# Optimization experiments

Hardware: AMD Instinct MI355X
Metric: run time of the kernel (lower is better)

The kernel has to match this reference:

```python
import jax, jax.numpy as jnp
import numpy as np

LEARNING_RATE = 0.1  # obj.learning_rate


def setup_inputs() -> dict:
    key = jax.random.key(0)
    k1, k2, k3, k4 = jax.random.split(key, 4)
    B, F = 50000, 100
    n_stages, n_classes, depth = 200, 10, 6
    T = n_stages * n_classes          # 2000 trees total
    n_internal = 2**depth - 1         # 63
    n_leaves = 2**depth               # 64
    x = jax.random.normal(k1, (B, F), dtype=jnp.float32)
    thresholds = jax.random.normal(k2, (T, n_internal), dtype=jnp.float32)
    leaf_values = jax.random.normal(k3, (T, n_leaves), dtype=jnp.float32)
    features = jax.random.randint(k4, (T, n_internal), 0, F, dtype=jnp.int32)
    classes = jnp.arange(n_classes, dtype=jnp.int64)
    return {"x": x, "thresholds": thresholds, "leaf_values": leaf_values,
            "features": features, "classes": classes}


def reference(x, thresholds, leaf_values, features, classes):
    # FIL-style batched traversal of complete depth-d trees.
    # Node i's children are 2i+1 (x[f] <= thr) and 2i+2 (x[f] > thr),
    # matching sklearn decision-tree split semantics.
    B = x.shape[0]
    T, n_internal = thresholds.shape
    n_leaves = leaf_values.shape[1]
    depth = int(np.log2(n_leaves))
    n_classes = classes.shape[0]

    tr = jnp.arange(T)[None, :]                      # [1, T] tree ids
    idx = jnp.zeros((B, T), dtype=jnp.int32)         # current node per (sample, tree)
    for _ in range(depth):                           # fixed small unroll (tree depth)
        f = features[tr, idx]                        # [B, T] split feature ids
        t = thresholds[tr, idx]                      # [B, T] split thresholds
        xv = jnp.take_along_axis(x, f, axis=1)       # [B, T] gathered feature values
        idx = 2 * idx + 1 + (xv > t).astype(jnp.int32)
    leaf = idx - (n_leaves - 1)                      # [B, T] leaf index in [0, n_leaves)
    vals = leaf_values[tr, leaf]                     # [B, T] per-tree outputs

    # stages-major layout: tree t = stage*n_classes + class; sum stages * lr
    # (init_ == 'zero' -> init output is zeros)
    decisions = LEARNING_RATE * vals.reshape(B, -1, n_classes).sum(axis=1)  # [B, C]
    # deviance, multiclass: predict_log_proba = log_softmax(decision_function)
    log_proba = jax.nn.log_softmax(decisions, axis=-1)
    # forward() = predict() = classes[argmax proba]; we return the float
    # log-probabilities (the differentiable hot path); argmax/class lookup is
    # a trivial epilogue: classes[jnp.argmax(log_proba, -1)]
    return log_proba
```

## Files before the change

kernel.cpp:

```cpp
#include <hip/hip_runtime.h>

#define B_SAMPLES 50000
#define F_FEATS   100
#define T_TREES   2000
#define N_INTERNAL 63
#define N_LEAVES  64
#define DEPTH     6
#define N_CLASSES 10
#define LR        0.1f

#define BLK 128
#define TPG 40
#define NCHUNK 10
#define TREES_PER_CHUNK (T_TREES / NCHUNK)
#define GROUPS_PER_CHUNK (TREES_PER_CHUNK / TPG)
#define NODE_STRIDE 64
#define NSB ((B_SAMPLES + BLK - 1) / BLK)

__global__ __launch_bounds__(256) void pack_nodes_kernel(
    const float* __restrict__ thresholds,
    const int*   __restrict__ features,
    int2*        __restrict__ nodes)
{
    int e = blockIdx.x * 256 + threadIdx.x;
    if (e < T_TREES * N_INTERNAL) {
        int t = e / N_INTERNAL;
        int i = e - t * N_INTERNAL;
        nodes[t * NODE_STRIDE + i] = make_int2(features[e], __float_as_int(thresholds[e]));
    }
}

#define I2F __int_as_float
#define XS(f) xs[((f) << 7) + tid]

template<bool PARTIALS>
__global__ __launch_bounds__(BLK, 1) void forest_kernel(
    const float* __restrict__ x,
    const int2*  __restrict__ nodes,
    const float* __restrict__ leaves,
    float*       __restrict__ accum)
{
    __shared__ float xs[F_FEATS * BLK];
    const int tid   = threadIdx.x;
    const int chunk = blockIdx.x % NCHUNK;
    const int sb    = blockIdx.x / NCHUNK;
    const int b     = sb * BLK + tid;
    const bool valid = (b < B_SAMPLES);

    {
        const float4* xrow = reinterpret_cast<const float4*>(x + (size_t)b * F_FEATS);
        #pragma unroll
        for (int k = 0; k < F_FEATS / 4; ++k) {
            float4 v = valid ? xrow[k] : make_float4(0.f, 0.f, 0.f, 0.f);
            xs[(4 * k + 0) * BLK + tid] = v.x;
            xs[(4 * k + 1) * BLK + tid] = v.y;
            xs[(4 * k + 2) * BLK + tid] = v.z;
            xs[(4 * k + 3) * BLK + tid] = v.w;
        }
    }
    __syncthreads();

    float acc[N_CLASSES];
    #pragma unroll
    for (int c = 0; c < N_CLASSES; ++c) acc[c] = 0.f;

    const int2*  cnodes  = nodes  + (size_t)chunk * TREES_PER_CHUNK * NODE_STRIDE;
    const float* cleaves = leaves + (size_t)chunk * TREES_PER_CHUNK * N_LEAVES;

    #pragma unroll 1
    for (int g = 0; g < GROUPS_PER_CHUNK; ++g) {
        const int2*  nbase = cnodes  + (size_t)g * TPG * NODE_STRIDE;
        const float* lbase = cleaves + (size_t)g * TPG * N_LEAVES;

        int idx[TPG];
        #pragma unroll
        for (int j = 0; j < TPG; ++j) idx[j] = 0;

        #pragma unroll
        for (int lvl = 0; lvl < DEPTH; ++lvl) {
            int2 nd[TPG];
            #pragma unroll
            for (int j = 0; j < TPG; ++j)
                nd[j] = nbase[j * NODE_STRIDE + idx[j]];
            #pragma unroll
            for (int j = 0; j < TPG; ++j) {
                float xv  = XS(nd[j].x);
                float thr = I2F(nd[j].y);
                idx[j] += idx[j] + 1 + (xv > thr ? 1 : 0);
            }
        }
        #pragma unroll
        for (int j = 0; j < TPG; ++j) {
            float lv = lbase[j * N_LEAVES + (idx[j] - (N_LEAVES - 1))];
            acc[j % N_CLASSES] += lv;
        }
    }

    if (valid) {
        if (PARTIALS) {
            float2* p = reinterpret_cast<float2*>(
                accum + ((size_t)chunk * B_SAMPLES + b) * N_CLASSES);
            #pragma unroll
            for (int c = 0; c < N_CLASSES / 2; ++c)
                p[c] = make_float2(acc[2 * c], acc[2 * c + 1]);
        } else {
            #pragma unroll
            for (int c = 0; c < N_CLASSES; ++c)
                atomicAdd(&accum[(size_t)b * N_CLASSES + c], acc[c]);
        }
    }
}

template<bool PARTIALS>
__global__ __launch_bounds__(256) void softmax_kernel(
    const float* __restrict__ accum,
    float*       __restrict__ out)
{
    int b = blockIdx.x * 256 + threadIdx.x;
    if (b >= B_SAMPLES) return;

    float d[N_CLASSES];
    #pragma unroll
    for (int c = 0; c < N_CLASSES; ++c) d[c] = 0.f;

    if (PARTIALS) {
        for (int ch = 0; ch < NCHUNK; ++ch) {
            const float2* p = reinterpret_cast<const float2*>(
                accum + ((size_t)ch * B_SAMPLES + b) * N_CLASSES);
            #pragma unroll
            for (int c = 0; c < N_CLASSES / 2; ++c) {
                float2 v = p[c];
                d[2 * c]     += v.x;
                d[2 * c + 1] += v.y;
            }
        }
    } else {
        #pragma unroll
        for (int c = 0; c < N_CLASSES; ++c)
            d[c] = accum[(size_t)b * N_CLASSES + c];
    }

    #pragma unroll
    for (int c = 0; c < N_CLASSES; ++c) d[c] *= LR;
    float m = d[0];
    #pragma unroll
    for (int c = 1; c < N_CLASSES; ++c) m = fmaxf(m, d[c]);
    float ssum = 0.f;
    #pragma unroll
    for (int c = 0; c < N_CLASSES; ++c) ssum += expf(d[c] - m);
    float lse = logf(ssum);

    float2* o = reinterpret_cast<float2*>(out + (size_t)b * N_CLASSES);
    #pragma unroll
    for (int c = 0; c < N_CLASSES / 2; ++c)
        o[c] = make_float2(d[2 * c] - m - lse, d[2 * c + 1] - m - lse);
}

extern "C" void kernel_launch(void* const* d_in, const int* in_sizes, int n_in,
                              void* d_out, int out_size, void* d_ws, size_t ws_size,
                              hipStream_t stream) {
    const float* x          = (const float*)d_in[0];
    const float* thresholds = (const float*)d_in[1];
    const float* leaves     = (const float*)d_in[2];
    const int*   features   = (const int*)d_in[3];

    const size_t nodes_bytes    = (size_t)T_TREES * NODE_STRIDE * sizeof(int2);
    const size_t partials_bytes = (size_t)NCHUNK * B_SAMPLES * N_CLASSES * sizeof(float);
    const size_t accum_bytes    = (size_t)B_SAMPLES * N_CLASSES * sizeof(float);

    int2*  nodes  = (int2*)d_ws;
    float* accbuf = (float*)((char*)d_ws + nodes_bytes);
    const bool use_partials = (ws_size >= nodes_bytes + partials_bytes);

    {
        int total = T_TREES * N_INTERNAL;
        pack_nodes_kernel<<<(total + 255) / 256, 256, 0, stream>>>(thresholds, features, nodes);
    }

    if (use_partials) {
        forest_kernel<true><<<NSB * NCHUNK, BLK, 0, stream>>>(x, nodes, leaves, accbuf);
        softmax_kernel<true><<<(B_SAMPLES + 255) / 256, 256, 0, stream>>>(accbuf, (float*)d_out);
    } else {
        hipMemsetAsync(accbuf, 0, accum_bytes, stream);
        forest_kernel<false><<<NSB * NCHUNK, BLK, 0, stream>>>(x, nodes, leaves, accbuf);
        softmax_kernel<false><<<(B_SAMPLES + 255) / 256, 256, 0, stream>>>(accbuf, (float*)d_out);
    }
}
```

Before: 402.2 us.

## Software-pipeline tree traversal across tree quarters and reorder block-to-chunk mapping

Halves the trees per group from 40 to 20 and splits them into four quarters of five. The traversal becomes a 24-step software pipeline: LDS reads of feature values for the next quarter are issued while the current quarter compares and issues its next global node or leaf load. Block indexing now puts the sample block in the fast dimension and the chunk in the slow one, so concurrently running blocks share the same tree chunk in cache. The aim is to hide global node-load and LDS latency, at the cost of more pipeline bookkeeping and less parallelism per group.

```diff
diff --git a/kernel.cpp b/kernel.cpp
--- a/kernel.cpp
+++ b/kernel.cpp
@@ -10,7 +10,8 @@
 #define LR        0.1f
 
 #define BLK 128
-#define TPG 40
+#define TPG 20
+#define QS  5
 #define NCHUNK 10
 #define TREES_PER_CHUNK (T_TREES / NCHUNK)
 #define GROUPS_PER_CHUNK (TREES_PER_CHUNK / TPG)
@@ -42,8 +43,8 @@
 {
     __shared__ float xs[F_FEATS * BLK];
     const int tid   = threadIdx.x;
-    const int chunk = blockIdx.x % NCHUNK;
-    const int sb    = blockIdx.x / NCHUNK;
+    const int chunk = blockIdx.x / NSB;
+    const int sb    = blockIdx.x % NSB;
     const int b     = sb * BLK + tid;
     const bool valid = (b < B_SAMPLES);
 
@@ -69,31 +70,47 @@
 
     #pragma unroll 1
     for (int g = 0; g < GROUPS_PER_CHUNK; ++g) {
-        const int2*  nbase = cnodes  + (size_t)g * TPG * NODE_STRIDE;
-        const float* lbase = cleaves + (size_t)g * TPG * N_LEAVES;
-
-        int idx[TPG];
+        const int2*  nb = cnodes  + (size_t)g * TPG * NODE_STRIDE;
+        const float* lb = cleaves + (size_t)g * TPG * N_LEAVES;
+
+        int   idx[TPG];
+        int2  nd [TPG];
+        float xv [TPG];
+        float lf [TPG];
+
         #pragma unroll
         for (int j = 0; j < TPG; ++j) idx[j] = 0;
-
-        #pragma unroll
-        for (int lvl = 0; lvl < DEPTH; ++lvl) {
-            int2 nd[TPG];
-            #pragma unroll
-            for (int j = 0; j < TPG; ++j)
-                nd[j] = nbase[j * NODE_STRIDE + idx[j]];
-            #pragma unroll
-            for (int j = 0; j < TPG; ++j) {
-                float xv  = XS(nd[j].x);
-                float thr = I2F(nd[j].y);
-                idx[j] += idx[j] + 1 + (xv > thr ? 1 : 0);
+        #pragma unroll
+        for (int j = 0; j < TPG; ++j) nd[j] = nb[j * NODE_STRIDE];
+        #pragma unroll
+        for (int jj = 0; jj < QS; ++jj) xv[jj] = XS(nd[jj].x);
+
+        #pragma unroll
+        for (int s = 0; s < 24; ++s) {
+            {
+                const int s1 = s + 1, q2 = s1 & 3, l2 = s1 >> 2, o2 = q2 * QS;
+                if (l2 <= 5) {
+                    #pragma unroll
+                    for (int jj = 0; jj < QS; ++jj) {
+                        const int j = o2 + jj;
+                        xv[j] = XS(nd[j].x);
+                    }
+                }
             }
-        }
-        #pragma unroll
-        for (int j = 0; j < TPG; ++j) {
-            float lv = lbase[j * N_LEAVES + (idx[j] - (N_LEAVES - 1))];
-            acc[j % N_CLASSES] += lv;
-        }
+            {
+                const int q = s & 3, l = s >> 2, o = q * QS;
+                #pragma unroll
+                for (int jj = 0; jj < QS; ++jj) {
+                    const int j = o + jj;
+                    idx[j] += idx[j] + 1 + (xv[j] > I2F(nd[j].y) ? 1 : 0);
+                    if (l < 5) nd[j] = nb[j * NODE_STRIDE + idx[j]];
+                    else       lf[j] = lb[j * N_LEAVES + idx[j] - (N_LEAVES - 1)];
+                }
+            }
+        }
+
+        #pragma unroll
+        for (int j = 0; j < TPG; ++j) acc[j % N_CLASSES] += lf[j];
     }
 
     if (valid) {
```

Measured after the change: 390.1 us. 3.0% less time.

## Split each block's tree chunk across four waves sharing the staged samples

Applied to the files above, without the earlier changes.

Each block now has 512 threads: four groups of 128 threads share the same 128 staged samples in LDS, and each group walks a quarter of the chunk's trees. The per-thread tree group shrinks from 40 to 10, which lowers register pressure and raises the number of resident waves for latency hiding. Per-class partial sums from the four groups are reduced through LDS before the write. This adds two barriers and an LDS reduction, and the x staging is divided among the groups. Occupancy may still be capped by the 51 KB LDS tile per block.

```diff
diff --git a/kernel.cpp b/kernel.cpp
--- a/kernel.cpp
+++ b/kernel.cpp
@@ -9,13 +9,17 @@
 #define N_CLASSES 10
 #define LR        0.1f
 
-#define BLK 128
-#define TPG 40
+#define SAMP 128
+#define NW   4
+#define THREADS (SAMP * NW)
+#define TPG 10
 #define NCHUNK 10
 #define TREES_PER_CHUNK (T_TREES / NCHUNK)
-#define GROUPS_PER_CHUNK (TREES_PER_CHUNK / TPG)
+#define TREES_PER_QUARTER (TREES_PER_CHUNK / NW)
+#define NGROUPS (TREES_PER_QUARTER / TPG)
 #define NODE_STRIDE 64
-#define NSB ((B_SAMPLES + BLK - 1) / BLK)
+#define NSB ((B_SAMPLES + SAMP - 1) / SAMP)
+#define RED_PAD 11
 
 __global__ __launch_bounds__(256) void pack_nodes_kernel(
     const float* __restrict__ thresholds,
@@ -31,31 +35,33 @@
 }
 
 #define I2F __int_as_float
-#define XS(f) xs[((f) << 7) + tid]
+#define XS(f) xs[((f) << 7) + s]
 
 template<bool PARTIALS>
-__global__ __launch_bounds__(BLK, 1) void forest_kernel(
+__global__ __launch_bounds__(THREADS, 1) void forest_kernel(
     const float* __restrict__ x,
     const int2*  __restrict__ nodes,
     const float* __restrict__ leaves,
     float*       __restrict__ accum)
 {
-    __shared__ float xs[F_FEATS * BLK];
+    __shared__ float xs[F_FEATS * SAMP];
     const int tid   = threadIdx.x;
+    const int s     = tid & (SAMP - 1);
+    const int w     = tid >> 7;
     const int chunk = blockIdx.x % NCHUNK;
     const int sb    = blockIdx.x / NCHUNK;
-    const int b     = sb * BLK + tid;
+    const int b     = sb * SAMP + s;
     const bool valid = (b < B_SAMPLES);
 
     {
         const float4* xrow = reinterpret_cast<const float4*>(x + (size_t)b * F_FEATS);
         #pragma unroll
-        for (int k = 0; k < F_FEATS / 4; ++k) {
+        for (int k = w; k < F_FEATS / 4; k += NW) {
             float4 v = valid ? xrow[k] : make_float4(0.f, 0.f, 0.f, 0.f);
-            xs[(4 * k + 0) * BLK + tid] = v.x;
-            xs[(4 * k + 1) * BLK + tid] = v.y;
-            xs[(4 * k + 2) * BLK + tid] = v.z;
-            xs[(4 * k + 3) * BLK + tid] = v.w;
+            xs[(4 * k + 0) * SAMP + s] = v.x;
+            xs[(4 * k + 1) * SAMP + s] = v.y;
+            xs[(4 * k + 2) * SAMP + s] = v.z;
+            xs[(4 * k + 3) * SAMP + s] = v.w;
         }
     }
     __syncthreads();
@@ -64,11 +70,13 @@
     #pragma unroll
     for (int c = 0; c < N_CLASSES; ++c) acc[c] = 0.f;
 
-    const int2*  cnodes  = nodes  + (size_t)chunk * TREES_PER_CHUNK * NODE_STRIDE;
-    const float* cleaves = leaves + (size_t)chunk * TREES_PER_CHUNK * N_LEAVES;
+    const int2*  cnodes  = nodes  + ((size_t)chunk * TREES_PER_CHUNK
+                                     + (size_t)w * TREES_PER_QUARTER) * NODE_STRIDE;
+    const float* cleaves = leaves + ((size_t)chunk * TREES_PER_CHUNK
+                                     + (size_t)w * TREES_PER_QUARTER) * N_LEAVES;
 
     #pragma unroll 1
-    for (int g = 0; g < GROUPS_PER_CHUNK; ++g) {
+    for (int g = 0; g < NGROUPS; ++g) {
         const int2*  nbase = cnodes  + (size_t)g * TPG * NODE_STRIDE;
         const float* lbase = cleaves + (size_t)g * TPG * N_LEAVES;
 
@@ -92,21 +100,39 @@
         #pragma unroll
         for (int j = 0; j < TPG; ++j) {
             float lv = lbase[j * N_LEAVES + (idx[j] - (N_LEAVES - 1))];
-            acc[j % N_CLASSES] += lv;
-        }
-    }
-
-    if (valid) {
+            acc[j] += lv;
+        }
+    }
+
+    __syncthreads();
+    {
+        float* red = xs;
+        #pragma unroll
+        for (int c = 0; c < N_CLASSES; ++c)
+            red[(w * SAMP + s) * RED_PAD + c] = acc[c];
+    }
+    __syncthreads();
+
+    if (w == 0 && valid) {
+        const float* red = xs;
+        float d[N_CLASSES];
+        #pragma unroll
+        for (int c = 0; c < N_CLASSES; ++c)
+            d[c] = red[s * RED_PAD + c]
+                 + red[(SAMP + s) * RED_PAD + c]
+                 + red[(2 * SAMP + s) * RED_PAD + c]
+                 + red[(3 * SAMP + s) * RED_PAD + c];
+
         if (PARTIALS) {
             float2* p = reinterpret_cast<float2*>(
                 accum + ((size_t)chunk * B_SAMPLES + b) * N_CLASSES);
             #pragma unroll
             for (int c = 0; c < N_CLASSES / 2; ++c)
-                p[c] = make_float2(acc[2 * c], acc[2 * c + 1]);
+                p[c] = make_float2(d[2 * c], d[2 * c + 1]);
         } else {
             #pragma unroll
             for (int c = 0; c < N_CLASSES; ++c)
-                atomicAdd(&accum[(size_t)b * N_CLASSES + c], acc[c]);
+                atomicAdd(&accum[(size_t)b * N_CLASSES + c], d[c]);
         }
     }
 }
@@ -178,11 +204,11 @@
     }
 
     if (use_partials) {
-        forest_kernel<true><<<NSB * NCHUNK, BLK, 0, stream>>>(x, nodes, leaves, accbuf);
+        forest_kernel<true><<<NSB * NCHUNK, THREADS, 0, stream>>>(x, nodes, leaves, accbuf);
         softmax_kernel<true><<<(B_SAMPLES + 255) / 256, 256, 0, stream>>>(accbuf, (float*)d_out);
     } else {
         hipMemsetAsync(accbuf, 0, accum_bytes, stream);
-        forest_kernel<false><<<NSB * NCHUNK, BLK, 0, stream>>>(x, nodes, leaves, accbuf);
+        forest_kernel<false><<<NSB * NCHUNK, THREADS, 0, stream>>>(x, nodes, leaves, accbuf);
         softmax_kernel<false><<<(B_SAMPLES + 255) / 256, 256, 0, stream>>>(accbuf, (float*)d_out);
     }
 }
```

Measured after the change: 409.2 us. No clear change (+1.7%).
